# Kernel tuning notes

Measured on AMD Instinct MI355X. Metric: run time of the kernel, lower is better.

Reference implementation:

```python
import jax, jax.numpy as jnp
import numpy as np

H = 4096  # input_size == hidden_size


def setup_inputs() -> dict:
    key = jax.random.key(0)
    ks = jax.random.split(key, 11)
    s = 1.0 / np.sqrt(2 * H)  # nn.Linear default init scale
    return {
        "h_tmin1": jax.random.normal(ks[0], (H,), jnp.float32),
        "c_tmin1": jax.random.normal(ks[1], (H,), jnp.float32),
        "x_t": jax.random.normal(ks[2], (H,), jnp.float32),
        "W_f": jax.random.uniform(ks[3], (H, 2 * H), jnp.float32, -s, s),
        "b_f": jax.random.uniform(ks[4], (H,), jnp.float32, -s, s),
        "W_i": jax.random.uniform(ks[5], (H, 2 * H), jnp.float32, -s, s),
        "b_i": jax.random.uniform(ks[6], (H,), jnp.float32, -s, s),
        "W_C": jax.random.uniform(ks[7], (H, 2 * H), jnp.float32, -s, s),
        "b_C": jax.random.uniform(ks[8], (H,), jnp.float32, -s, s),
        "W_o": jax.random.uniform(ks[9], (H, 2 * H), jnp.float32, -s, s),
        "b_o": jax.random.uniform(ks[10], (H,), jnp.float32, -s, s),
    }


def reference(h_tmin1, c_tmin1, x_t, W_f, b_f, W_i, b_i, W_C, b_C, W_o, b_o):
    # z_hx = cat([h, x]) used for f, i, o gates.
    z_hx = jnp.concatenate([h_tmin1, x_t])          # [2H]
    # Faithful quirk: original C_t calls Ctilde_t(h_tmin1, c_tmin1),
    # so the candidate gate sees cat([h, c]) instead of cat([h, x]).
    z_hc = jnp.concatenate([h_tmin1, c_tmin1])      # [2H]

    f = jax.nn.sigmoid(W_f @ z_hx + b_f)            # forget gate  [H]
    i = jax.nn.sigmoid(W_i @ z_hx + b_i)            # input gate   [H]
    Ctilde = jnp.tanh(W_C @ z_hc + b_C)             # candidate    [H]
    C = f * c_tmin1 + i * Ctilde                    # new cell     [H]
    o = jax.nn.sigmoid(W_o @ z_hx + b_o)            # output gate  [H]
    h = o * jnp.tanh(C)                             # new hidden   [H]
    # output() returns (hidden, cell); it recomputes C_t redundantly in the
    # original, which is mathematically identical to reusing C here.
    return (h, C)
```

## Files before the change

kernel.cpp:

```cpp
#include <hip/hip_runtime.h>
#include <math.h>

constexpr int H  = 4096;
constexpr int H2 = 8192;

typedef float f32x4 __attribute__((ext_vector_type(4)));

__device__ __forceinline__ float dot4s(const f32x4 w, const f32x4 v) {
    return fmaf(w.x, v.x, fmaf(w.y, v.y, fmaf(w.z, v.z, w.w * v.w)));
}

__global__ __launch_bounds__(256, 4)
void lstm_step_kernel(const float* __restrict__ h_prev,
                      const float* __restrict__ c_prev,
                      const float* __restrict__ x_t,
                      const float* __restrict__ W_f, const float* __restrict__ b_f,
                      const float* __restrict__ W_i, const float* __restrict__ b_i,
                      const float* __restrict__ W_C, const float* __restrict__ b_C,
                      const float* __restrict__ W_o, const float* __restrict__ b_o,
                      float* __restrict__ out)
{
    const int gtid = blockIdx.x * blockDim.x + threadIdx.x;
    const int row  = gtid >> 6;
    const int lane = threadIdx.x & 63;
    if (row >= H) return;

    const f32x4* wf = (const f32x4*)(W_f + (size_t)row * H2);
    const f32x4* wi = (const f32x4*)(W_i + (size_t)row * H2);
    const f32x4* wc = (const f32x4*)(W_C + (size_t)row * H2);
    const f32x4* wo = (const f32x4*)(W_o + (size_t)row * H2);
    const f32x4* hv = (const f32x4*)h_prev;
    const f32x4* xv = (const f32x4*)x_t;
    const f32x4* cv = (const f32x4*)c_prev;

    float sf = 0.f, si = 0.f, sc = 0.f, so = 0.f;

    for (int it = 0; it < 16; ++it) {
        const int c = it * 64 + lane;
        const f32x4 z = hv[c];
        const f32x4 a = wf[c];
        const f32x4 b = __builtin_nontemporal_load(wi + c);
        const f32x4 d = wc[c];
        const f32x4 e = __builtin_nontemporal_load(wo + c);
        sf += dot4s(a, z);
        si += dot4s(b, z);
        sc += dot4s(d, z);
        so += dot4s(e, z);
    }

    for (int it = 0; it < 16; ++it) {
        const int c = it * 64 + lane;
        const int w = 1024 + c;
        const f32x4 zx = xv[c];
        const f32x4 zc = cv[c];
        const f32x4 a = wf[w];
        const f32x4 b = __builtin_nontemporal_load(wi + w);
        const f32x4 d = wc[w];
        const f32x4 e = __builtin_nontemporal_load(wo + w);
        sf += dot4s(a, zx);
        si += dot4s(b, zx);
        sc += dot4s(d, zc);
        so += dot4s(e, zx);
    }

    #pragma unroll
    for (int off = 32; off > 0; off >>= 1) {
        sf += __shfl_down(sf, off, 64);
        si += __shfl_down(si, off, 64);
        sc += __shfl_down(sc, off, 64);
        so += __shfl_down(so, off, 64);
    }

    if (lane == 0) {
        const float f      = 1.f / (1.f + expf(-(sf + b_f[row])));
        const float ig     = 1.f / (1.f + expf(-(si + b_i[row])));
        const float ctilde = tanhf(sc + b_C[row]);
        const float og     = 1.f / (1.f + expf(-(so + b_o[row])));
        const float Cnew   = f * c_prev[row] + ig * ctilde;
        out[row]     = og * tanhf(Cnew);
        out[H + row] = Cnew;
    }
}

extern "C" void kernel_launch(void* const* d_in, const int* in_sizes, int n_in,
                              void* d_out, int out_size, void* d_ws, size_t ws_size,
                              hipStream_t stream) {
    const float* h_prev = (const float*)d_in[0];
    const float* c_prev = (const float*)d_in[1];
    const float* x_t    = (const float*)d_in[2];
    const float* W_f    = (const float*)d_in[3];
    const float* b_f    = (const float*)d_in[4];
    const float* W_i    = (const float*)d_in[5];
    const float* b_i    = (const float*)d_in[6];
    const float* W_C    = (const float*)d_in[7];
    const float* b_C    = (const float*)d_in[8];
    const float* W_o    = (const float*)d_in[9];
    const float* b_o    = (const float*)d_in[10];
    float* out = (float*)d_out;

    lstm_step_kernel<<<(H * 64) / 256, 256, 0, stream>>>(
        h_prev, c_prev, x_t, W_f, b_f, W_i, b_i, W_C, b_C, W_o, b_o, out);
}
```

Measured before the change: 81.20 us.

## Split gate dot products across wavefronts, one row per block

Each block now handles a single output row, and each of its four wavefronts computes the dot product for one gate. The partial sums are combined through shared memory before thread 0 applies the activations. This gives each wave one weight stream instead of four, which cuts register pressure and raises the requested occupancy. In exchange it adds a block barrier and launches four times as many blocks, while the total memory traffic stays the same.

```diff
diff --git a/kernel.cpp b/kernel.cpp
--- a/kernel.cpp
+++ b/kernel.cpp
@@ -10,7 +10,7 @@
     return fmaf(w.x, v.x, fmaf(w.y, v.y, fmaf(w.z, v.z, w.w * v.w)));
 }
 
-__global__ __launch_bounds__(256, 4)
+__global__ __launch_bounds__(256, 8)
 void lstm_step_kernel(const float* __restrict__ h_prev,
                       const float* __restrict__ c_prev,
                       const float* __restrict__ x_t,
@@ -20,62 +20,52 @@
                       const float* __restrict__ W_o, const float* __restrict__ b_o,
                       float* __restrict__ out)
 {
-    const int gtid = blockIdx.x * blockDim.x + threadIdx.x;
-    const int row  = gtid >> 6;
+    __shared__ float part[4];
+
+    const int row  = blockIdx.x;
+    const int wid  = threadIdx.x >> 6;
     const int lane = threadIdx.x & 63;
-    if (row >= H) return;
 
-    const f32x4* wf = (const f32x4*)(W_f + (size_t)row * H2);
-    const f32x4* wi = (const f32x4*)(W_i + (size_t)row * H2);
-    const f32x4* wc = (const f32x4*)(W_C + (size_t)row * H2);
-    const f32x4* wo = (const f32x4*)(W_o + (size_t)row * H2);
+    const float* Wg = (wid == 0) ? W_f : (wid == 1) ? W_i
+                    : (wid == 2) ? W_C : W_o;
+    const f32x4* wg = (const f32x4*)(Wg + (size_t)row * H2);
     const f32x4* hv = (const f32x4*)h_prev;
-    const f32x4* xv = (const f32x4*)x_t;
-    const f32x4* cv = (const f32x4*)c_prev;
+    const f32x4* z2 = (wid == 2) ? (const f32x4*)c_prev : (const f32x4*)x_t;
 
-    float sf = 0.f, si = 0.f, sc = 0.f, so = 0.f;
+    float s = 0.f;
 
-    for (int it = 0; it < 16; ++it) {
-        const int c = it * 64 + lane;
-        const f32x4 z = hv[c];
-        const f32x4 a = wf[c];
-        const f32x4 b = __builtin_nontemporal_load(wi + c);
-        const f32x4 d = wc[c];
-        const f32x4 e = __builtin_nontemporal_load(wo + c);
-        sf += dot4s(a, z);
-        si += dot4s(b, z);
-        sc += dot4s(d, z);
-        so += dot4s(e, z);
-    }
-
-    for (int it = 0; it < 16; ++it) {
-        const int c = it * 64 + lane;
-        const int w = 1024 + c;
-        const f32x4 zx = xv[c];
-        const f32x4 zc = cv[c];
-        const f32x4 a = wf[w];
-        const f32x4 b = __builtin_nontemporal_load(wi + w);
-        const f32x4 d = wc[w];
-        const f32x4 e = __builtin_nontemporal_load(wo + w);
-        sf += dot4s(a, zx);
-        si += dot4s(b, zx);
-        sc += dot4s(d, zc);
-        so += dot4s(e, zx);
+    if ((wid & 1) == 0) {
+        for (int it = 0; it < 16; ++it) {
+            const int c = it * 64 + lane;
+            s += dot4s(wg[c], hv[c]);
+        }
+        for (int it = 0; it < 16; ++it) {
+            const int c = it * 64 + lane;
+            s += dot4s(wg[1024 + c], z2[c]);
+        }
+    } else {
+        for (int it = 0; it < 16; ++it) {
+            const int c = it * 64 + lane;
+            s += dot4s(__builtin_nontemporal_load(wg + c), hv[c]);
+        }
+        for (int it = 0; it < 16; ++it) {
+            const int c = it * 64 + lane;
+            s += dot4s(__builtin_nontemporal_load(wg + 1024 + c), z2[c]);
+        }
     }
 
     #pragma unroll
-    for (int off = 32; off > 0; off >>= 1) {
-        sf += __shfl_down(sf, off, 64);
-        si += __shfl_down(si, off, 64);
-        sc += __shfl_down(sc, off, 64);
-        so += __shfl_down(so, off, 64);
-    }
+    for (int off = 32; off > 0; off >>= 1)
+        s += __shfl_down(s, off, 64);
 
-    if (lane == 0) {
-        const float f      = 1.f / (1.f + expf(-(sf + b_f[row])));
-        const float ig     = 1.f / (1.f + expf(-(si + b_i[row])));
-        const float ctilde = tanhf(sc + b_C[row]);
-        const float og     = 1.f / (1.f + expf(-(so + b_o[row])));
+    if (lane == 0) part[wid] = s;
+    __syncthreads();
+
+    if (threadIdx.x == 0) {
+        const float f      = 1.f / (1.f + expf(-(part[0] + b_f[row])));
+        const float ig     = 1.f / (1.f + expf(-(part[1] + b_i[row])));
+        const float ctilde = tanhf(part[2] + b_C[row]);
+        const float og     = 1.f / (1.f + expf(-(part[3] + b_o[row])));
         const float Cnew   = f * c_prev[row] + ig * ctilde;
         out[row]     = og * tanhf(Cnew);
         out[H + row] = Cnew;
@@ -98,6 +88,6 @@
     const float* b_o    = (const float*)d_in[10];
     float* out = (float*)d_out;
 
-    lstm_step_kernel<<<(H * 64) / 256, 256, 0, stream>>>(
+    lstm_step_kernel<<<H, 256, 0, stream>>>(
         h_prev, c_prev, x_t, W_f, b_f, W_i, b_i, W_C, b_C, W_o, b_o, out);
 }
```

Result: slower. 122.7 us (+51.1%).
